# Performance work log

Hardware: AMD Instinct MI355X
Metric: run time of the kernel (lower is better)

The kernel has to match this reference:

```python
import jax, jax.numpy as jnp
import numpy as np

ALPHA = 0.1
NUM_CLASSES = 10000
FEAT_DIM = 256
BATCH = 8192


def setup_inputs() -> dict:
    key = jax.random.key(0)
    k1, k2, k3 = jax.random.split(key, 3)
    feat = jax.random.normal(k1, (BATCH, FEAT_DIM), dtype=jnp.float32)
    label = jax.random.randint(k2, (BATCH,), 0, NUM_CLASSES, dtype=jnp.int64)
    # centers parameter, initialized ~ randn as in the torch constructor
    centers = jax.random.normal(k3, (NUM_CLASSES, FEAT_DIM), dtype=jnp.float32)
    return {"feat": feat, "label": label, "centers": centers}


def reference(feat, label, centers):
    B = feat.shape[0]
    # dist[b,c] = ||feat[b] - centers[c]||^2, computed in GEMM form:
    # ||f||^2 + ||c||^2 - 2 f.c  (same math as the broadcast diff^2 sum)
    f_sq = jnp.sum(feat * feat, axis=-1, keepdims=True)          # [B, 1]
    c_sq = jnp.sum(centers * centers, axis=-1)[None, :]          # [1, C]
    cross = jnp.einsum('bd,cd->bc', feat, centers)               # [B, C]
    dist = f_sq + c_sq - 2.0 * cross                             # [B, C]

    # one-hot margin scaling: y_onehot = alpha * onehot(label) + 1
    onehot = jax.nn.one_hot(label, NUM_CLASSES, dtype=dist.dtype)  # [B, C]
    margin_dist = dist * (onehot * ALPHA + 1.0)

    margin_logits = -0.5 * margin_dist
    logits = -0.5 * dist

    # likelihood: mean over batch of 0.5 * ||feat - centers[label]||^2
    cdiff = feat - centers[label]                                 # [B, D]
    likelihood = jnp.sum(cdiff * cdiff) / (2.0 * B)
    return (logits, margin_logits, likelihood)
```

## Files before the change

kernel.cpp:

```cpp
#include <hip/hip_runtime.h>
#include <hip/hip_bf16.h>


#define ALPHA_ 0.1f
constexpr int BATCH = 8192;
constexpr int NCLS  = 10000;
constexpr int FDIM  = 256;

typedef __attribute__((ext_vector_type(8))) short bf16x8;
typedef __attribute__((ext_vector_type(4))) float f32x4;

__device__ __forceinline__ unsigned short f2bf(float f) {
  unsigned int u = __float_as_uint(f);
  u += 0x7FFF + ((u >> 16) & 1);
  return (unsigned short)(u >> 16);
}

__global__ void prep_kernel(const float* __restrict__ feat,
                            const float* __restrict__ centers,
                            unsigned short* __restrict__ fbf,
                            unsigned short* __restrict__ cbf,
                            float* __restrict__ fsq,
                            float* __restrict__ csq) {
  int gw = (int)((blockIdx.x * blockDim.x + threadIdx.x) >> 6);
  int lane = threadIdx.x & 63;
  if (gw >= BATCH + NCLS) return;
  const float* src; unsigned short* dst; float* sq;
  if (gw < BATCH) {
    src = feat + (size_t)gw * FDIM; dst = fbf + (size_t)gw * FDIM; sq = fsq + gw;
  } else {
    int r = gw - BATCH;
    src = centers + (size_t)r * FDIM; dst = cbf + (size_t)r * FDIM; sq = csq + r;
  }
  float4 v = reinterpret_cast<const float4*>(src)[lane];
  ushort4 b;
  b.x = f2bf(v.x); b.y = f2bf(v.y); b.z = f2bf(v.z); b.w = f2bf(v.w);
  reinterpret_cast<ushort4*>(dst)[lane] = b;
  float s = v.x*v.x + v.y*v.y + v.z*v.z + v.w*v.w;
  #pragma unroll
  for (int off = 32; off >= 1; off >>= 1) s += __shfl_xor(s, off, 64);
  if (lane == 0) *sq = s;
}

#define BM 128
#define BN 128
#define BK 64
#define BROWS 144

__global__ __launch_bounds__(512, 4)
void gemm_kernel(const unsigned short* __restrict__ fbf,
                 const unsigned short* __restrict__ cbf,
                 const float* __restrict__ fsq,
                 const float* __restrict__ csq,
                 const int* __restrict__ label,
                 float* __restrict__ out_logits,
                 float* __restrict__ out_margin,
                 float* __restrict__ lik_row) {
  __shared__ unsigned short As[2][BM * BK];
  __shared__ unsigned short Bs[2][BROWS * BK];

  const int NTN = (NCLS + BN - 1) / BN;
  const int NWG = (BATCH / BM) * NTN;

  int bid = blockIdx.x;
  int wg = (bid & 7) * (NWG >> 3) + (bid >> 3);
  int mt = wg / NTN;
  int nt = wg - mt * NTN;

  const int tid  = threadIdx.x;
  const int lane = tid & 63;
  const int wid  = tid >> 6;
  const int wr   = (wid >> 2) * 64;
  const int wc   = (wid & 3) * 32;
  const int sr   = tid >> 3;
  const int sc   = tid & 7;
  const int mloc  = wr + (lane & 15);

  const size_t a_base = (size_t)(mt * BM) * FDIM;
  const int c0 = nt * BN;

  f32x4 acc[4][3];
  #pragma unroll
  for (int i = 0; i < 4; i++)
    #pragma unroll
    for (int j = 0; j < 3; j++) acc[i][j] = (f32x4){0.f, 0.f, 0.f, 0.f};

  bf16x8 va[2], vb[2], vbh;

  #define LOADT(k0_) do {                                                      \
    _Pragma("unroll")                                                          \
    for (int j = 0; j < 2; ++j) {                                              \
      int r = j * 64 + sr;                                                     \
      va[j] = *reinterpret_cast<const bf16x8*>(fbf + a_base + (size_t)r * FDIM + (k0_) + sc * 8); \
      int cc = c0 + r; cc = (cc < NCLS) ? cc : (NCLS - 1);                     \
      vb[j] = *reinterpret_cast<const bf16x8*>(cbf + (size_t)cc * FDIM + (k0_) + sc * 8); \
    }                                                                          \
    if (tid < 128) {                                                           \
      int ch_ = c0 - 16 + (tid >> 3); ch_ = (ch_ >= 0) ? ch_ : 0;              \
      vbh = *reinterpret_cast<const bf16x8*>(cbf + (size_t)ch_ * FDIM + (k0_) + sc * 8); \
    }                                                                          \
  } while (0)

  #define STORET(b_) do {                                                      \
    _Pragma("unroll")                                                          \
    for (int j = 0; j < 2; ++j) {                                              \
      int r = j * 64 + sr;                                                     \
      int offa = r * BK + ((sc ^ (r & 7)) * 8);                                \
      *reinterpret_cast<bf16x8*>(&As[b_][offa]) = va[j];                       \
      int rb = r + 16;                                                         \
      int offb = rb * BK + ((sc ^ (rb & 7)) * 8);                              \
      *reinterpret_cast<bf16x8*>(&Bs[b_][offb]) = vb[j];                       \
    }                                                                          \
    if (tid < 128) {                                                           \
      int rh = tid >> 3;                                                       \
      int offh = rh * BK + ((sc ^ (rh & 7)) * 8);                              \
      *reinterpret_cast<bf16x8*>(&Bs[b_][offh]) = vbh;                         \
    }                                                                          \
  } while (0)

  LOADT(0);
  STORET(0);

  #pragma unroll
  for (int kc = 0; kc < FDIM / BK; ++kc) {
    const int cur = kc & 1;
    if (kc < FDIM / BK - 1) LOADT((kc + 1) * BK);
    __syncthreads();
    #pragma unroll
    for (int kk = 0; kk < BK / 32; ++kk) {
      const int ch = kk * 4 + (lane >> 4);
      bf16x8 a[4], b[3];
      #pragma unroll
      for (int i = 0; i < 4; i++) {
        int row = wr + i * 16 + (lane & 15);
        a[i] = *reinterpret_cast<const bf16x8*>(&As[cur][row * BK + ((ch ^ (row & 7)) * 8)]);
      }
      #pragma unroll
      for (int j = 0; j < 3; j++) {
        int row = wc + j * 16 + (lane & 15);
        b[j] = *reinterpret_cast<const bf16x8*>(&Bs[cur][row * BK + ((ch ^ (row & 7)) * 8)]);
      }
      #pragma unroll
      for (int i = 0; i < 4; i++)
        #pragma unroll
        for (int j = 0; j < 3; j++)
          acc[i][j] = __builtin_amdgcn_mfma_f32_16x16x32_bf16(b[j], a[i], acc[i][j], 0, 0, 0);
    }
    if (kc < FDIM / BK - 1) STORET(cur ^ 1);
  }

  const int p = lane & 1;
  #pragma unroll
  for (int i = 0; i < 4; i++) {
    int m = mt * BM + mloc + i * 16;
    float fs = fsq[m];
    int lb = label[m];
    size_t rowoff = (size_t)m * NCLS;
    #pragma unroll
    for (int j = 0; j < 3; j++) {
      if (p ? (j >= 2) : (j == 0)) continue;
      int n0 = c0 + wc + (j - 1) * 16 + ((lane >> 4) << 2);
      if (n0 < 0 || n0 >= NCLS) continue;
      float4 cs = *reinterpret_cast<const float4*>(&csq[n0]);
      f32x4 v = acc[i][j];
      f32x4 lg;
      lg[0] = v[0] - 0.5f * (fs + cs.x);
      lg[1] = v[1] - 0.5f * (fs + cs.y);
      lg[2] = v[2] - 0.5f * (fs + cs.z);
      lg[3] = v[3] - 0.5f * (fs + cs.w);
      *reinterpret_cast<f32x4*>(&out_logits[rowoff + n0]) = lg;
      f32x4 mg;
      mg[0] = (lb == n0    ) ? lg[0] * (1.0f + ALPHA_) : lg[0];
      mg[1] = (lb == n0 + 1) ? lg[1] * (1.0f + ALPHA_) : lg[1];
      mg[2] = (lb == n0 + 2) ? lg[2] * (1.0f + ALPHA_) : lg[2];
      mg[3] = (lb == n0 + 3) ? lg[3] * (1.0f + ALPHA_) : lg[3];
      *reinterpret_cast<f32x4*>(&out_margin[rowoff + n0]) = mg;
      if (lb >= n0 && lb < n0 + 4) {
        float lv = (lb == n0) ? lg[0] : (lb == n0 + 1) ? lg[1]
                 : (lb == n0 + 2) ? lg[2] : lg[3];
        lik_row[m] = -lv;
      }
    }
  }
  #undef LOADT
  #undef STORET
}

__global__ void lik_reduce_kernel(const float* __restrict__ lik_row,
                                  float* __restrict__ out) {
  int t = threadIdx.x;
  float v = 0.f;
  #pragma unroll
  for (int i = 0; i < BATCH / 1024; i++) v += lik_row[t + i * 1024];
  #pragma unroll
  for (int off = 32; off >= 1; off >>= 1) v += __shfl_xor(v, off, 64);
  __shared__ float red[16];
  if ((t & 63) == 0) red[t >> 6] = v;
  __syncthreads();
  if (t == 0) {
    float s = 0.f;
    #pragma unroll
    for (int i = 0; i < 16; i++) s += red[i];
    out[0] = s * (1.0f / BATCH);
  }
}

extern "C" void kernel_launch(void* const* d_in, const int* in_sizes, int n_in,
                              void* d_out, int out_size, void* d_ws, size_t ws_size,
                              hipStream_t stream) {
  const float* feat    = (const float*)d_in[0];
  const int*   label   = (const int*)d_in[1];
  const float* centers = (const float*)d_in[2];

  float* out        = (float*)d_out;
  float* out_logits = out;
  float* out_margin = out + (size_t)BATCH * NCLS;
  float* out_lik    = out + 2 * (size_t)BATCH * NCLS;

  char* ws = (char*)d_ws;
  unsigned short* fbf = (unsigned short*)ws;
  unsigned short* cbf = (unsigned short*)(ws + (size_t)BATCH * FDIM * 2);
  float* fsq     = (float*)(ws + (size_t)BATCH * FDIM * 2 + (size_t)NCLS * FDIM * 2);
  float* csq     = fsq + BATCH;
  float* lik_row = csq + NCLS;

  prep_kernel<<<(BATCH + NCLS) / 4, 256, 0, stream>>>(feat, centers, fbf, cbf, fsq, csq);
  gemm_kernel<<<(BATCH / BM) * ((NCLS + BN - 1) / BN), 512, 0, stream>>>(
      fbf, cbf, fsq, csq, label, out_logits, out_margin, lik_row);
  lik_reduce_kernel<<<1, 1024, 0, stream>>>(lik_row, out_lik);
}
```

Baseline: 198.0 us.

## Stage GEMM epilogue through LDS for fully coalesced output row stores

The epilogue now writes computed logits tiles into a shared-memory buffer that is unioned with the A/B staging buffers. It then re-reads them so each group of 32 threads stores a contiguous 128-float row segment of logits and margin outputs. The aim is to make the write-dominated output traffic (two 8192x10000 fp32 matrices) coalesced instead of scattered 16-byte pieces from the MFMA layout. The cost is extra LDS traffic, additional __syncthreads, two serialized half-tile passes, and a possible occupancy change from the larger shared footprint.

```diff
diff --git a/kernel.cpp b/kernel.cpp
--- a/kernel.cpp
+++ b/kernel.cpp
@@ -46,6 +46,7 @@
 #define BN 128
 #define BK 64
 #define BROWS 144
+#define CTS 148
 
 __global__ __launch_bounds__(512, 4)
 void gemm_kernel(const unsigned short* __restrict__ fbf,
@@ -56,8 +57,10 @@
                  float* __restrict__ out_logits,
                  float* __restrict__ out_margin,
                  float* __restrict__ lik_row) {
-  __shared__ unsigned short As[2][BM * BK];
-  __shared__ unsigned short Bs[2][BROWS * BK];
+  __shared__ union SMem {
+    struct { unsigned short A[2][BM * BK]; unsigned short B[2][BROWS * BK]; } ab;
+    float ct[64 * CTS];
+  } sm;
 
   const int NTN = (NCLS + BN - 1) / BN;
   const int NWG = (BATCH / BM) * NTN;
@@ -74,7 +77,6 @@
   const int wc   = (wid & 3) * 32;
   const int sr   = tid >> 3;
   const int sc   = tid & 7;
-  const int mloc  = wr + (lane & 15);
 
   const size_t a_base = (size_t)(mt * BM) * FDIM;
   const int c0 = nt * BN;
@@ -106,15 +108,15 @@
     for (int j = 0; j < 2; ++j) {                                              \
       int r = j * 64 + sr;                                                     \
       int offa = r * BK + ((sc ^ (r & 7)) * 8);                                \
-      *reinterpret_cast<bf16x8*>(&As[b_][offa]) = va[j];                       \
+      *reinterpret_cast<bf16x8*>(&sm.ab.A[b_][offa]) = va[j];                  \
       int rb = r + 16;                                                         \
       int offb = rb * BK + ((sc ^ (rb & 7)) * 8);                              \
-      *reinterpret_cast<bf16x8*>(&Bs[b_][offb]) = vb[j];                       \
+      *reinterpret_cast<bf16x8*>(&sm.ab.B[b_][offb]) = vb[j];                  \
     }                                                                          \
     if (tid < 128) {                                                           \
       int rh = tid >> 3;                                                       \
       int offh = rh * BK + ((sc ^ (rh & 7)) * 8);                              \
-      *reinterpret_cast<bf16x8*>(&Bs[b_][offh]) = vbh;                         \
+      *reinterpret_cast<bf16x8*>(&sm.ab.B[b_][offh]) = vbh;                    \
     }                                                                          \
   } while (0)
 
@@ -133,12 +135,12 @@
       #pragma unroll
       for (int i = 0; i < 4; i++) {
         int row = wr + i * 16 + (lane & 15);
-        a[i] = *reinterpret_cast<const bf16x8*>(&As[cur][row * BK + ((ch ^ (row & 7)) * 8)]);
+        a[i] = *reinterpret_cast<const bf16x8*>(&sm.ab.A[cur][row * BK + ((ch ^ (row & 7)) * 8)]);
       }
       #pragma unroll
       for (int j = 0; j < 3; j++) {
         int row = wc + j * 16 + (lane & 15);
-        b[j] = *reinterpret_cast<const bf16x8*>(&Bs[cur][row * BK + ((ch ^ (row & 7)) * 8)]);
+        b[j] = *reinterpret_cast<const bf16x8*>(&sm.ab.B[cur][row * BK + ((ch ^ (row & 7)) * 8)]);
       }
       #pragma unroll
       for (int i = 0; i < 4; i++)
@@ -148,39 +150,59 @@
     }
     if (kc < FDIM / BK - 1) STORET(cur ^ 1);
   }
-
-  const int p = lane & 1;
-  #pragma unroll
-  for (int i = 0; i < 4; i++) {
-    int m = mt * BM + mloc + i * 16;
-    float fs = fsq[m];
-    int lb = label[m];
-    size_t rowoff = (size_t)m * NCLS;
-    #pragma unroll
-    for (int j = 0; j < 3; j++) {
-      if (p ? (j >= 2) : (j == 0)) continue;
-      int n0 = c0 + wc + (j - 1) * 16 + ((lane >> 4) << 2);
+  __syncthreads();
+
+  #pragma unroll
+  for (int chk = 0; chk < 2; ++chk) {
+    if ((wid >> 2) == chk) {
+      #pragma unroll
+      for (int i = 0; i < 4; i++) {
+        int rr = i * 16 + (lane & 15);
+        int m  = mt * BM + chk * 64 + rr;
+        float fs = fsq[m];
+        #pragma unroll
+        for (int j = 0; j < 3; j++) {
+          int wcol = wc + (j - 1) * 16 + ((lane >> 4) << 2) + 16;
+          int col  = c0 - 16 + wcol;
+          int ccl  = (col < 0) ? 0 : ((col > NCLS - 4) ? (NCLS - 4) : col);
+          float4 cs = *reinterpret_cast<const float4*>(&csq[ccl]);
+          f32x4 v = acc[i][j];
+          f32x4 lg;
+          lg[0] = v[0] - 0.5f * (fs + cs.x);
+          lg[1] = v[1] - 0.5f * (fs + cs.y);
+          lg[2] = v[2] - 0.5f * (fs + cs.z);
+          lg[3] = v[3] - 0.5f * (fs + cs.w);
+          *reinterpret_cast<f32x4*>(&sm.ct[rr * CTS + wcol]) = lg;
+        }
+      }
+    }
+    __syncthreads();
+    #pragma unroll
+    for (int it = 0; it < 4; ++it) {
+      int rr = it * 16 + (tid >> 5);
+      int p  = rr & 1;
+      int cidx = (tid & 31) << 2;
+      int widx = (p ? 0 : 16) + cidx;
+      int n0 = c0 - (p ? 16 : 0) + cidx;
       if (n0 < 0 || n0 >= NCLS) continue;
-      float4 cs = *reinterpret_cast<const float4*>(&csq[n0]);
-      f32x4 v = acc[i][j];
-      f32x4 lg;
-      lg[0] = v[0] - 0.5f * (fs + cs.x);
-      lg[1] = v[1] - 0.5f * (fs + cs.y);
-      lg[2] = v[2] - 0.5f * (fs + cs.z);
-      lg[3] = v[3] - 0.5f * (fs + cs.w);
-      *reinterpret_cast<f32x4*>(&out_logits[rowoff + n0]) = lg;
+      int m  = mt * BM + chk * 64 + rr;
+      f32x4 lg = *reinterpret_cast<const f32x4*>(&sm.ct[rr * CTS + widx]);
+      size_t idx = (size_t)m * NCLS + n0;
+      *reinterpret_cast<f32x4*>(&out_logits[idx]) = lg;
+      int lb = label[m];
       f32x4 mg;
       mg[0] = (lb == n0    ) ? lg[0] * (1.0f + ALPHA_) : lg[0];
       mg[1] = (lb == n0 + 1) ? lg[1] * (1.0f + ALPHA_) : lg[1];
       mg[2] = (lb == n0 + 2) ? lg[2] * (1.0f + ALPHA_) : lg[2];
       mg[3] = (lb == n0 + 3) ? lg[3] * (1.0f + ALPHA_) : lg[3];
-      *reinterpret_cast<f32x4*>(&out_margin[rowoff + n0]) = mg;
+      *reinterpret_cast<f32x4*>(&out_margin[idx]) = mg;
       if (lb >= n0 && lb < n0 + 4) {
         float lv = (lb == n0) ? lg[0] : (lb == n0 + 1) ? lg[1]
                  : (lb == n0 + 2) ? lg[2] : lg[3];
         lik_row[m] = -lv;
       }
     }
+    __syncthreads();
   }
   #undef LOADT
   #undef STORET
```

New measurement: 234.5 us. +18.4%, slower.
